# Performance work log

Measured on AMD Instinct MI355X. Metric: run time of the kernel, lower is better.

## Reference

```python
import jax, jax.numpy as jnp
import numpy as np

TOPK = 0.1  # fraction of h*w spatial positions, from __init__ default


def setup_inputs() -> dict:
    key = jax.random.key(0)
    x = jax.random.normal(key, (32, 256, 56, 56), dtype=jnp.float32)
    return {"x": x}


def reference(x) -> jnp.ndarray:
    # Faithful translation of TopKLayer.sparse_hw (including its quirky
    # comparison of ascending *ranks* against the spatial *index* of the
    # k-th largest element, exactly as the torch code does).
    n, c, h, w = x.shape
    k = int(max(1, TOPK * h * w))  # topk_keep_num = 313 for 56x56
    x_r = x.reshape(n * c, h * w)              # (nc, hw)
    abs_x = jnp.abs(x_r)
    # ranks[i, j] = ascending rank of abs_x[i, j] within row i
    ranks = jnp.argsort(jnp.argsort(abs_x, axis=1), axis=1)
    # spatial index of the k-th largest |x| in each row
    thr_idx = jax.lax.top_k(abs_x, k)[1][:, -1]  # (nc,)
    mask = (ranks < thr_idx[:, None]).reshape(n, c, h, w)
    return x * mask.astype(x.dtype)
```

## Files before the change

### kernel.cpp

```cpp
#include <hip/hip_runtime.h>
#include <stdint.h>


#define HW    3136
#define NW4   784
#define NT    256
#define KSEL  313u
#define CAP   320
#define CAP2  64
#define O_CAND 0
#define O_HC   384
#define O_TINY 704

__device__ __forceinline__ unsigned wscan(unsigned v) {
    const int lane = threadIdx.x & 63;
#pragma unroll
    for (int d = 1; d < 64; d <<= 1) {
        unsigned o = __shfl_up(v, d, 64);
        if (lane >= d) v += o;
    }
    return v;
}

template <bool fromTop>
__device__ unsigned select_finish(const uint4* s_x4, unsigned* s_h,
                                  unsigned* s_warp, unsigned* s_b,
                                  unsigned b0, unsigned m1) {
    const int t = threadIdx.x;
    const int lane = t & 63;
    const int wid = t >> 6;
    unsigned* cand = s_h + O_CAND;

    for (int j = t; j < NW4; j += NT) {
        uint4 v = s_x4[j];
        const unsigned i0 = 4u * (unsigned)j;
        unsigned k, p;
        k = v.x & 0x7fffffffu;
        if ((k >> 20) == b0) { p = atomicAdd(&s_b[3], 1u); if (p < CAP) cand[p] = ((k & 0xFFFFFu) << 12) | i0; }
        k = v.y & 0x7fffffffu;
        if ((k >> 20) == b0) { p = atomicAdd(&s_b[3], 1u); if (p < CAP) cand[p] = ((k & 0xFFFFFu) << 12) | (i0 + 1u); }
        k = v.z & 0x7fffffffu;
        if ((k >> 20) == b0) { p = atomicAdd(&s_b[3], 1u); if (p < CAP) cand[p] = ((k & 0xFFFFFu) << 12) | (i0 + 2u); }
        k = v.w & 0x7fffffffu;
        if ((k >> 20) == b0) { p = atomicAdd(&s_b[3], 1u); if (p < CAP) cand[p] = ((k & 0xFFFFFu) << 12) | (i0 + 3u); }
    }
    __syncthreads();
    const unsigned cnt = s_b[3];
    bool fb = (cnt > CAP);

    if (!fb) {
        unsigned* hc = s_h + O_HC;
        hc[t] = 0;
        if (t == 0) s_b[5] = 0;
        __syncthreads();
        for (int i = t; i < (int)cnt; i += NT) atomicAdd(&hc[cand[i] >> 24], 1u);
        __syncthreads();
        const unsigned sc = hc[t];
        unsigned Sic = wscan(sc);
        if (lane == 63) s_warp[wid] = Sic;
        __syncthreads();
        unsigned crossc = 0;
        for (int w2 = 0; w2 < wid; ++w2) crossc += s_warp[w2];
        const unsigned cdf2 = crossc + Sic - sc;
        bool hit;
        unsigned m2c = 0;
        if (fromTop) {
            const unsigned suf2 = cnt - cdf2 - sc;
            hit = (suf2 < m1 && m1 <= suf2 + sc);
            if (hit) m2c = m1 - suf2;
        } else {
            hit = (cdf2 < m1 && m1 <= cdf2 + sc);
            if (hit) m2c = m1 - cdf2;
        }
        if (hit) { s_b[0] = (unsigned)t; s_b[1] = m2c; }
        __syncthreads();
        const unsigned b2 = s_b[0];
        const unsigned m2 = s_b[1];
        unsigned* tiny = s_h + O_TINY;
        for (int i = t; i < (int)cnt; i += NT) {
            const unsigned cc = cand[i];
            if ((cc >> 24) == b2) { const unsigned p = atomicAdd(&s_b[5], 1u); if (p < CAP2) tiny[p] = cc; }
        }
        __syncthreads();
        const unsigned c2 = s_b[5];
        if (c2 > CAP2) fb = true;
        else {
            if (t < (int)c2) {
                const unsigned ci = tiny[t];
                const unsigned di = fromTop ? (ci ^ 0xFFFu) : ci;
                unsigned r = 1;
                for (unsigned j = 0; j < c2; ++j) {
                    const unsigned dj = fromTop ? (tiny[j] ^ 0xFFFu) : tiny[j];
                    if (fromTop ? (dj > di) : (dj < di)) r++;
                }
                if (r == m2) s_b[2] = ci;
            }
            __syncthreads();
        }
    }

    if (fb) {
        const unsigned* s_x = (const unsigned*)s_x4;
        for (int j = t; j < HW; j += NT) {
            const unsigned k = s_x[j] & 0x7fffffffu;
            if ((k >> 20) != b0) continue;
            unsigned Ci = ((k & 0xFFFFFu) << 12) | (unsigned)j;
            if (fromTop) Ci ^= 0xFFFu;
            unsigned r = 1;
            for (int j2 = 0; j2 < HW; ++j2) {
                const unsigned k2 = s_x[j2] & 0x7fffffffu;
                if ((k2 >> 20) != b0) continue;
                unsigned Cj = ((k2 & 0xFFFFFu) << 12) | (unsigned)j2;
                if (fromTop) Cj ^= 0xFFFu;
                if (fromTop ? (Cj > Ci) : (Cj < Ci)) r++;
            }
            if (r == m1) s_b[2] = ((k & 0xFFFFFu) << 12) | (unsigned)j;
        }
        __syncthreads();
    }
    return s_b[2];
}

extern "C" __global__ void __launch_bounds__(NT)
topk_kernel(const float* __restrict__ x, float* __restrict__ out) {
    __shared__ uint4 s_x4[NW4];
    __shared__ uint4 s_h4[512];
    __shared__ unsigned s_warp[4];
    __shared__ unsigned s_b[8];
    unsigned* s_h = (unsigned*)s_h4;

    const int t = threadIdx.x;
    const int lane = t & 63;
    const int wid = t >> 6;
    const int row = blockIdx.x;
    const uint4* __restrict__ xin = (const uint4*)(x + (size_t)row * HW);
    uint4* __restrict__ xout = (uint4*)(out + (size_t)row * HW);

    {
        uint4 z = make_uint4(0u, 0u, 0u, 0u);
        s_h4[t] = z;
        s_h4[t + NT] = z;
    }
    __syncthreads();
    for (int j = t; j < NW4; j += NT) {
        uint4 v = xin[j];
        s_x4[j] = v;
        atomicAdd(&s_h[(v.x & 0x7fffffffu) >> 20], 1u);
        atomicAdd(&s_h[(v.y & 0x7fffffffu) >> 20], 1u);
        atomicAdd(&s_h[(v.z & 0x7fffffffu) >> 20], 1u);
        atomicAdd(&s_h[(v.w & 0x7fffffffu) >> 20], 1u);
    }
    __syncthreads();

    const uint4 ca = s_h4[2 * t];
    const uint4 cb = s_h4[2 * t + 1];
    unsigned c[8] = {ca.x, ca.y, ca.z, ca.w, cb.x, cb.y, cb.z, cb.w};
    unsigned pre[8];
    unsigned ssum = 0;
#pragma unroll
    for (int i = 0; i < 8; ++i) { pre[i] = ssum; ssum += c[i]; }
    unsigned Si = wscan(ssum);
    if (lane == 63) s_warp[wid] = Si;
    __syncthreads();
    unsigned cross = 0;
    for (int w2 = 0; w2 < wid; ++w2) cross += s_warp[w2];
    const unsigned base = cross + Si - ssum;

    if (t == 0) s_b[3] = 0;
#pragma unroll
    for (int i = 0; i < 8; ++i) {
        const unsigned cdfb = base + pre[i];
        const unsigned suf = HW - cdfb - c[i];
        if (suf < KSEL && KSEL <= suf + c[i]) {
            s_b[0] = 8u * (unsigned)t + (unsigned)i;
            s_b[1] = KSEL - suf;
        }
    }
    __syncthreads();
    const unsigned b0A = s_b[0];
    const unsigned m1A = s_b[1];
    const unsigned compA = select_finish<true>(s_x4, s_h, s_warp, s_b, b0A, m1A);
    const unsigned tIdx = compA & 0xFFFu;

    if (tIdx == 0) {
        uint4 z = make_uint4(0u, 0u, 0u, 0u);
        for (int j = t; j < NW4; j += NT) xout[j] = z;
        return;
    }

    if (t == 0) s_b[3] = 0;
#pragma unroll
    for (int i = 0; i < 8; ++i) {
        const unsigned cdfb = base + pre[i];
        if (cdfb < tIdx && tIdx <= cdfb + c[i]) {
            s_b[0] = 8u * (unsigned)t + (unsigned)i;
            s_b[1] = tIdx - cdfb;
        }
    }
    __syncthreads();
    const unsigned b0B = s_b[0];
    const unsigned m1B = s_b[1];
    const unsigned compB = select_finish<false>(s_x4, s_h, s_warp, s_b, b0B, m1B);
    const unsigned KB = (b0B << 20) | (compB >> 12);
    const unsigned eB = compB & 0xFFFu;

    for (int j = t; j < NW4; j += NT) {
        uint4 v = s_x4[j];
        const unsigned i0 = 4u * (unsigned)j;
        unsigned k;
        k = v.x & 0x7fffffffu; if (!(k < KB || (k == KB && i0      <= eB))) v.x = 0u;
        k = v.y & 0x7fffffffu; if (!(k < KB || (k == KB && i0 + 1u <= eB))) v.y = 0u;
        k = v.z & 0x7fffffffu; if (!(k < KB || (k == KB && i0 + 2u <= eB))) v.z = 0u;
        k = v.w & 0x7fffffffu; if (!(k < KB || (k == KB && i0 + 3u <= eB))) v.w = 0u;
        xout[j] = v;
    }
}

extern "C" void kernel_launch(void* const* d_in, const int* in_sizes, int n_in,
                              void* d_out, int out_size, void* d_ws, size_t ws_size,
                              hipStream_t stream) {
    const float* x = (const float*)d_in[0];
    float* out = (float*)d_out;
    const int rows = in_sizes[0] / HW;
    topk_kernel<<<dim3(rows), dim3(NT), 0, stream>>>(x, out);
}
```

Before: 62.92 us.

## Keep row values in registers instead of shared memory staging

Each thread now loads its four uint4 chunks of the row into registers and reuses them for the histogram, both candidate-collection passes and the final masking. The 12.5 KB shared-memory copy of the row goes away, and the rare fallback path reads global memory directly. This cuts LDS traffic and LDS footprint per block, which may allow more resident blocks per CU. In exchange it raises register pressure. The second-level histogram reset is also reordered so it reuses an existing barrier, dropping one sync.

Result: no change. 62.80 us (-0.2%).

```diff
diff --git a/kernel.cpp b/kernel.cpp
--- a/kernel.cpp
+++ b/kernel.cpp
@@ -23,47 +23,52 @@
 }
 
 template <bool fromTop>
-__device__ unsigned select_finish(const uint4* s_x4, unsigned* s_h,
-                                  unsigned* s_warp, unsigned* s_b,
+__device__ unsigned select_finish(uint4 v0, uint4 v1, uint4 v2, uint4 v3, bool has3,
+                                  const unsigned* __restrict__ gx,
+                                  unsigned* s_h, unsigned* s_warp, unsigned* s_b,
                                   unsigned b0, unsigned m1) {
     const int t = threadIdx.x;
     const int lane = t & 63;
     const int wid = t >> 6;
     unsigned* cand = s_h + O_CAND;
-
-    for (int j = t; j < NW4; j += NT) {
-        uint4 v = s_x4[j];
-        const unsigned i0 = 4u * (unsigned)j;
-        unsigned k, p;
-        k = v.x & 0x7fffffffu;
-        if ((k >> 20) == b0) { p = atomicAdd(&s_b[3], 1u); if (p < CAP) cand[p] = ((k & 0xFFFFFu) << 12) | i0; }
-        k = v.y & 0x7fffffffu;
-        if ((k >> 20) == b0) { p = atomicAdd(&s_b[3], 1u); if (p < CAP) cand[p] = ((k & 0xFFFFFu) << 12) | (i0 + 1u); }
-        k = v.z & 0x7fffffffu;
-        if ((k >> 20) == b0) { p = atomicAdd(&s_b[3], 1u); if (p < CAP) cand[p] = ((k & 0xFFFFFu) << 12) | (i0 + 2u); }
-        k = v.w & 0x7fffffffu;
-        if ((k >> 20) == b0) { p = atomicAdd(&s_b[3], 1u); if (p < CAP) cand[p] = ((k & 0xFFFFFu) << 12) | (i0 + 3u); }
+    unsigned* hc   = s_h + O_HC;
+
+    {
+        auto put = [&](unsigned w, unsigned idx) {
+            const unsigned k = w & 0x7fffffffu;
+            if ((k >> 20) == b0) {
+                const unsigned p = atomicAdd(&s_b[3], 1u);
+                if (p < CAP) cand[p] = ((k & 0xFFFFFu) << 12) | idx;
+            }
+        };
+        unsigned i0 = 4u * (unsigned)t;
+        put(v0.x, i0); put(v0.y, i0 + 1u); put(v0.z, i0 + 2u); put(v0.w, i0 + 3u);
+        i0 = 4u * (unsigned)(t + NT);
+        put(v1.x, i0); put(v1.y, i0 + 1u); put(v1.z, i0 + 2u); put(v1.w, i0 + 3u);
+        i0 = 4u * (unsigned)(t + 2 * NT);
+        put(v2.x, i0); put(v2.y, i0 + 1u); put(v2.z, i0 + 2u); put(v2.w, i0 + 3u);
+        if (has3) {
+            i0 = 4u * (unsigned)(t + 3 * NT);
+            put(v3.x, i0); put(v3.y, i0 + 1u); put(v3.z, i0 + 2u); put(v3.w, i0 + 3u);
+        }
     }
     __syncthreads();
     const unsigned cnt = s_b[3];
     bool fb = (cnt > CAP);
 
     if (!fb) {
-        unsigned* hc = s_h + O_HC;
+        for (int i = t; i < (int)cnt; i += NT) atomicAdd(&hc[cand[i] >> 24], 1u);
+        __syncthreads();
+        const unsigned sc = hc[t];
+        const unsigned Sic = wscan(sc);
+        if (lane == 63) s_warp[wid] = Sic;
         hc[t] = 0;
         if (t == 0) s_b[5] = 0;
-        __syncthreads();
-        for (int i = t; i < (int)cnt; i += NT) atomicAdd(&hc[cand[i] >> 24], 1u);
-        __syncthreads();
-        const unsigned sc = hc[t];
-        unsigned Sic = wscan(sc);
-        if (lane == 63) s_warp[wid] = Sic;
         __syncthreads();
         unsigned crossc = 0;
         for (int w2 = 0; w2 < wid; ++w2) crossc += s_warp[w2];
         const unsigned cdf2 = crossc + Sic - sc;
-        bool hit;
-        unsigned m2c = 0;
+        bool hit; unsigned m2c = 0;
         if (fromTop) {
             const unsigned suf2 = cnt - cdf2 - sc;
             hit = (suf2 < m1 && m1 <= suf2 + sc);
@@ -100,15 +105,14 @@
     }
 
     if (fb) {
-        const unsigned* s_x = (const unsigned*)s_x4;
         for (int j = t; j < HW; j += NT) {
-            const unsigned k = s_x[j] & 0x7fffffffu;
+            const unsigned k = gx[j] & 0x7fffffffu;
             if ((k >> 20) != b0) continue;
             unsigned Ci = ((k & 0xFFFFFu) << 12) | (unsigned)j;
             if (fromTop) Ci ^= 0xFFFu;
             unsigned r = 1;
             for (int j2 = 0; j2 < HW; ++j2) {
-                const unsigned k2 = s_x[j2] & 0x7fffffffu;
+                const unsigned k2 = gx[j2] & 0x7fffffffu;
                 if ((k2 >> 20) != b0) continue;
                 unsigned Cj = ((k2 & 0xFFFFFu) << 12) | (unsigned)j2;
                 if (fromTop) Cj ^= 0xFFFu;
@@ -123,11 +127,9 @@
 
 extern "C" __global__ void __launch_bounds__(NT)
 topk_kernel(const float* __restrict__ x, float* __restrict__ out) {
-    __shared__ uint4 s_x4[NW4];
-    __shared__ uint4 s_h4[512];
+    __shared__ unsigned s_h[2048];
     __shared__ unsigned s_warp[4];
     __shared__ unsigned s_b[8];
-    unsigned* s_h = (unsigned*)s_h4;
 
     const int t = threadIdx.x;
     const int lane = t & 63;
@@ -135,38 +137,56 @@
     const int row = blockIdx.x;
     const uint4* __restrict__ xin = (const uint4*)(x + (size_t)row * HW);
     uint4* __restrict__ xout = (uint4*)(out + (size_t)row * HW);
+    const unsigned* __restrict__ gx = (const unsigned*)xin;
 
     {
-        uint4 z = make_uint4(0u, 0u, 0u, 0u);
-        s_h4[t] = z;
-        s_h4[t + NT] = z;
-    }
-    __syncthreads();
-    for (int j = t; j < NW4; j += NT) {
-        uint4 v = xin[j];
-        s_x4[j] = v;
-        atomicAdd(&s_h[(v.x & 0x7fffffffu) >> 20], 1u);
-        atomicAdd(&s_h[(v.y & 0x7fffffffu) >> 20], 1u);
-        atomicAdd(&s_h[(v.z & 0x7fffffffu) >> 20], 1u);
-        atomicAdd(&s_h[(v.w & 0x7fffffffu) >> 20], 1u);
-    }
-    __syncthreads();
-
-    const uint4 ca = s_h4[2 * t];
-    const uint4 cb = s_h4[2 * t + 1];
+        const uint4 z = make_uint4(0u, 0u, 0u, 0u);
+        ((uint4*)s_h)[t] = z;
+        ((uint4*)s_h)[t + NT] = z;
+    }
+    __syncthreads();
+
+    const bool has3 = (t < NW4 - 3 * NT);
+    const uint4 v0 = xin[t];
+    const uint4 v1 = xin[t + NT];
+    const uint4 v2 = xin[t + 2 * NT];
+    const uint4 v3 = has3 ? xin[t + 3 * NT] : make_uint4(0u, 0u, 0u, 0u);
+    atomicAdd(&s_h[(v0.x & 0x7fffffffu) >> 20], 1u);
+    atomicAdd(&s_h[(v0.y & 0x7fffffffu) >> 20], 1u);
+    atomicAdd(&s_h[(v0.z & 0x7fffffffu) >> 20], 1u);
+    atomicAdd(&s_h[(v0.w & 0x7fffffffu) >> 20], 1u);
+    atomicAdd(&s_h[(v1.x & 0x7fffffffu) >> 20], 1u);
+    atomicAdd(&s_h[(v1.y & 0x7fffffffu) >> 20], 1u);
+    atomicAdd(&s_h[(v1.z & 0x7fffffffu) >> 20], 1u);
+    atomicAdd(&s_h[(v1.w & 0x7fffffffu) >> 20], 1u);
+    atomicAdd(&s_h[(v2.x & 0x7fffffffu) >> 20], 1u);
+    atomicAdd(&s_h[(v2.y & 0x7fffffffu) >> 20], 1u);
+    atomicAdd(&s_h[(v2.z & 0x7fffffffu) >> 20], 1u);
+    atomicAdd(&s_h[(v2.w & 0x7fffffffu) >> 20], 1u);
+    if (has3) {
+        atomicAdd(&s_h[(v3.x & 0x7fffffffu) >> 20], 1u);
+        atomicAdd(&s_h[(v3.y & 0x7fffffffu) >> 20], 1u);
+        atomicAdd(&s_h[(v3.z & 0x7fffffffu) >> 20], 1u);
+        atomicAdd(&s_h[(v3.w & 0x7fffffffu) >> 20], 1u);
+    }
+    __syncthreads();
+
+    const uint4 ca = ((const uint4*)s_h)[2 * t];
+    const uint4 cb = ((const uint4*)s_h)[2 * t + 1];
     unsigned c[8] = {ca.x, ca.y, ca.z, ca.w, cb.x, cb.y, cb.z, cb.w};
     unsigned pre[8];
     unsigned ssum = 0;
 #pragma unroll
     for (int i = 0; i < 8; ++i) { pre[i] = ssum; ssum += c[i]; }
-    unsigned Si = wscan(ssum);
+    const unsigned Si = wscan(ssum);
     if (lane == 63) s_warp[wid] = Si;
     __syncthreads();
     unsigned cross = 0;
     for (int w2 = 0; w2 < wid; ++w2) cross += s_warp[w2];
     const unsigned base = cross + Si - ssum;
 
-    if (t == 0) s_b[3] = 0;
+    s_h[O_HC + t] = 0;
+    if (t == 0) { s_b[3] = 0; s_b[5] = 0; }
 #pragma unroll
     for (int i = 0; i < 8; ++i) {
         const unsigned cdfb = base + pre[i];
@@ -179,16 +199,18 @@
     __syncthreads();
     const unsigned b0A = s_b[0];
     const unsigned m1A = s_b[1];
-    const unsigned compA = select_finish<true>(s_x4, s_h, s_warp, s_b, b0A, m1A);
+    const unsigned compA =
+        select_finish<true>(v0, v1, v2, v3, has3, gx, s_h, s_warp, s_b, b0A, m1A);
     const unsigned tIdx = compA & 0xFFFu;
 
     if (tIdx == 0) {
-        uint4 z = make_uint4(0u, 0u, 0u, 0u);
-        for (int j = t; j < NW4; j += NT) xout[j] = z;
+        const uint4 z = make_uint4(0u, 0u, 0u, 0u);
+        xout[t] = z; xout[t + NT] = z; xout[t + 2 * NT] = z;
+        if (has3) xout[t + 3 * NT] = z;
         return;
     }
 
-    if (t == 0) s_b[3] = 0;
+    if (t == 0) { s_b[3] = 0; s_b[5] = 0; }
 #pragma unroll
     for (int i = 0; i < 8; ++i) {
         const unsigned cdfb = base + pre[i];
@@ -200,19 +222,35 @@
     __syncthreads();
     const unsigned b0B = s_b[0];
     const unsigned m1B = s_b[1];
-    const unsigned compB = select_finish<false>(s_x4, s_h, s_warp, s_b, b0B, m1B);
+    const unsigned compB =
+        select_finish<false>(v0, v1, v2, v3, has3, gx, s_h, s_warp, s_b, b0B, m1B);
     const unsigned KB = (b0B << 20) | (compB >> 12);
     const unsigned eB = compB & 0xFFFu;
 
-    for (int j = t; j < NW4; j += NT) {
-        uint4 v = s_x4[j];
-        const unsigned i0 = 4u * (unsigned)j;
-        unsigned k;
-        k = v.x & 0x7fffffffu; if (!(k < KB || (k == KB && i0      <= eB))) v.x = 0u;
-        k = v.y & 0x7fffffffu; if (!(k < KB || (k == KB && i0 + 1u <= eB))) v.y = 0u;
-        k = v.z & 0x7fffffffu; if (!(k < KB || (k == KB && i0 + 2u <= eB))) v.z = 0u;
-        k = v.w & 0x7fffffffu; if (!(k < KB || (k == KB && i0 + 3u <= eB))) v.w = 0u;
-        xout[j] = v;
+    {
+        auto msk = [&](unsigned w, unsigned idx) -> unsigned {
+            const unsigned k = w & 0x7fffffffu;
+            return (k < KB || (k == KB && idx <= eB)) ? w : 0u;
+        };
+        uint4 o;
+        unsigned i0 = 4u * (unsigned)t;
+        o.x = msk(v0.x, i0); o.y = msk(v0.y, i0 + 1u);
+        o.z = msk(v0.z, i0 + 2u); o.w = msk(v0.w, i0 + 3u);
+        xout[t] = o;
+        i0 = 4u * (unsigned)(t + NT);
+        o.x = msk(v1.x, i0); o.y = msk(v1.y, i0 + 1u);
+        o.z = msk(v1.z, i0 + 2u); o.w = msk(v1.w, i0 + 3u);
+        xout[t + NT] = o;
+        i0 = 4u * (unsigned)(t + 2 * NT);
+        o.x = msk(v2.x, i0); o.y = msk(v2.y, i0 + 1u);
+        o.z = msk(v2.z, i0 + 2u); o.w = msk(v2.w, i0 + 3u);
+        xout[t + 2 * NT] = o;
+        if (has3) {
+            i0 = 4u * (unsigned)(t + 3 * NT);
+            o.x = msk(v3.x, i0); o.y = msk(v3.y, i0 + 1u);
+            o.z = msk(v3.z, i0 + 2u); o.w = msk(v3.w, i0 + 3u);
+            xout[t + 3 * NT] = o;
+        }
     }
 }
 
```
